# Kernel tuning notes

Measured on AMD Instinct MI355X. Metric: run time of the kernel, lower is better.

The kernel has to match this reference:

```python
import jax, jax.numpy as jnp
import numpy as np

N, E, M = 20000, 320000, 64
LOG2 = float(np.log(2.0))
INV_SQRT_M = 1.0 / float(np.sqrt(M))
PW_S = float(np.sqrt(1.0 / 5.0))   # path weight for 0e-output paths: sqrt(ir_out.dim / n_paths)
PW_V = float(np.sqrt(3.0 / 5.0))   # path weight for 1e-output paths
INV_SQRT3 = 1.0 / float(np.sqrt(3.0))
INV_SQRT2 = 1.0 / float(np.sqrt(2.0))


def ssp(x):  # ShiftedSoftPlus
    return jax.nn.softplus(x) - LOG2


def split(feat):
    return feat[:, :M], feat[:, M:].reshape(feat.shape[0], M, 3)


def e3_linear(feat, W0, b0, W1):
    # e3nn o3.Linear per irrep group, fan-in normalized; bias only on scalar (0e) irreps
    s, v = split(feat)
    s = s @ (W0 * INV_SQRT_M) + b0
    v = jnp.einsum('nui,uv->nvi', v, W1 * INV_SQRT_M)
    return jnp.concatenate([s, v.reshape(v.shape[0], 3 * M)], axis=-1)


def fcnet(h, Ws):
    # e3nn FullyConnectedNet: no biases, fan-in normalized, ssp between layers
    for i, W in enumerate(Ws):
        h = h @ (W * (1.0 / float(np.sqrt(W.shape[0]))))
        if i < len(Ws) - 1:
            h = ssp(h)
    return h


def setup_inputs() -> dict:
    key = jax.random.key(0)
    ks = jax.random.split(key, 24)
    r = lambda i, shape: jax.random.normal(ks[i], shape, dtype=jnp.float32)
    inp = {
        'x': r(0, (N, 4 * M)),
        'edge_index': jax.random.randint(ks[1], (2, E), 0, N, dtype=jnp.int64)
        if jax.config.jax_enable_x64 else jax.random.randint(ks[1], (2, E), 0, N),
        'edge_sh': r(2, (E, 4)),
        'edge_attr': r(3, (E, 64)),
        # linear_node_pre
        'W_pre0': r(4, (M, M)), 'b_pre0': jnp.zeros((M,), jnp.float32), 'W_pre1': r(5, (M, M)),
        # NormGate fc (plain torch nn.Linear with bias)
        'Wg1': r(6, (2 * M, 2 * M)) * 0.08, 'bg1': jnp.zeros((2 * M,), jnp.float32),
        'Wg2': r(7, (2 * M, 2 * M)) * 0.08, 'bg2': jnp.zeros((2 * M,), jnp.float32),
        # linear_node
        'Wn0': r(8, (M, M)), 'bn0': jnp.zeros((M,), jnp.float32), 'Wn1': r(9, (M, M)),
        # fc_node: [edge_attr_dim=64, 32, weight_numel=5*M]
        'Wf1': r(10, (64, 32)), 'Wf2': r(11, (32, 5 * M)),
        # layer_l0: [192, 32, 5*M]
        'Wl1': r(12, (192, 32)), 'Wl2': r(13, (32, 5 * M)),
        # linear_out
        'Wo0': r(14, (M, M)), 'bo0': jnp.zeros((M,), jnp.float32), 'Wo1': r(15, (M, M)),
    }
    return inp


def reference(x, edge_index, edge_sh, edge_attr,
              W_pre0, b_pre0, W_pre1, Wg1, bg1, Wg2, bg2,
              Wn0, bn0, Wn1, Wf1, Wf2, Wl1, Wl2, Wo0, bo0, Wo1):
    edge_dst, edge_src = edge_index[0], edge_index[1]

    # --- pre linear + edge invariants s0 ---
    pre_x = e3_linear(x, W_pre0, b_pre0, W_pre1)
    ps, pv = split(pre_x)
    # InnerProduct on 1e group (uuu, path weight 1/ir.dim): mean over m of elementwise product
    ip1 = jnp.einsum('eui,eui->eu', pv[edge_dst], pv[edge_src]) * (1.0 / 3.0)  # [E, M]
    s0 = jnp.concatenate([ps[edge_dst], ps[edge_dst], ip1], axis=-1)  # [E, 192]

    # --- NormGate ---
    xs, xv = split(x)
    norm_v = jnp.sqrt(jnp.sum(xv * xv, axis=-1) + 1e-12)  # [N, M]
    f0 = jnp.concatenate([xs, norm_v], axis=-1)  # [N, 2M]
    g = jax.nn.silu(f0 @ Wg1 + bg1) @ Wg2 + bg2  # [N, 2M]
    gated = xv * g[:, M:, None]
    xg = jnp.concatenate([g[:, :M], gated.reshape(N, 3 * M)], axis=-1)

    xg = e3_linear(xg, Wn0, bn0, Wn1)
    self_x = xg

    # --- per-edge tensor product weights ---
    w = (fcnet(edge_attr, [Wf1, Wf2]) * fcnet(s0, [Wl1, Wl2])).reshape(E, 5, M)

    # --- edge-wise equivariant tensor product (uvu, 5 paths) ---
    gs, gv = split(xg)
    es, ev = gs[edge_src], gv[edge_src]            # [E,M], [E,M,3]
    sh0, sh1 = edge_sh[:, 0], edge_sh[:, 1:4]      # [E], [E,3]

    out_s = PW_S * (w[:, 0] * es * sh0[:, None]
                    + w[:, 3] * jnp.einsum('eui,ei->eu', ev, sh1) * INV_SQRT3)
    cross = jnp.cross(ev, sh1[:, None, :])
    out_v = PW_V * (w[:, 1][:, :, None] * es[:, :, None] * sh1[:, None, :]
                    + w[:, 2][:, :, None] * ev * sh0[:, None, None]
                    + w[:, 4][:, :, None] * cross * INV_SQRT2)
    edge_feat = jnp.concatenate([out_s, out_v.reshape(E, 3 * M)], axis=-1)  # [E, 4M]

    # --- scatter aggregate to destination nodes ---
    out = jax.ops.segment_sum(edge_feat, edge_dst, num_segments=N)
    out = out + self_x  # irrep_in_node == irrep_out
    out = e3_linear(out, Wo0, bo0, Wo1)
    return out
```

## Files before the change

kernel.cpp:

```cpp
#include <hip/hip_runtime.h>
#include <math.h>

#define NNODE 20000
#define NEDGE 320000

__device__ __forceinline__ float sspf(float x) {
    return fmaxf(x, 0.f) + log1pf(expf(-fabsf(x))) - 0.6931471805599453f;
}

__device__ __forceinline__ float rl(float v, int l) {
    return __int_as_float(__builtin_amdgcn_readlane(__float_as_int(v), l));
}

__global__ __launch_bounds__(256) void k_e3lin(
    const float* __restrict__ in, const float* __restrict__ add,
    float* __restrict__ out,
    const float* __restrict__ W0, const float* __restrict__ b0,
    const float* __restrict__ W1, int nrows)
{
    __shared__ float sW0[64 * 64];
    __shared__ float sW1[64 * 64];
    __shared__ float sb0[64];
    __shared__ float srow[4][256];
    const int tid = threadIdx.x;
    for (int i = tid; i < 64 * 16; i += 256) {
        ((float4*)sW0)[i] = ((const float4*)W0)[i];
        ((float4*)sW1)[i] = ((const float4*)W1)[i];
    }
    if (tid < 64) sb0[tid] = b0[tid];
    __syncthreads();

    const int rr = tid >> 6;
    const int v  = tid & 63;
    for (int r0 = blockIdx.x * 4; r0 < nrows; r0 += gridDim.x * 4) {
        {
            int i = tid;
            int r = i >> 6, c = i & 63;
            int row = r0 + r;
            float4 val = make_float4(0.f, 0.f, 0.f, 0.f);
            if (row < nrows) {
                val = ((const float4*)(in + (size_t)row * 256))[c];
                if (add) {
                    float4 a = ((const float4*)(add + (size_t)row * 256))[c];
                    val.x += a.x; val.y += a.y; val.z += a.z; val.w += a.w;
                }
            }
            ((float4*)srow[r])[c] = val;
        }
        __syncthreads();

        int row = r0 + rr;
        if (row < nrows) {
            const float* rw = srow[rr];
            float s = 0.f, a0 = 0.f, a1 = 0.f, a2 = 0.f;
            #pragma unroll 16
            for (int u = 0; u < 64; ++u) {
                float w0 = sW0[u * 64 + v];
                float w1 = sW1[u * 64 + v];
                s  += rw[u] * w0;
                a0 += rw[64 + u * 3 + 0] * w1;
                a1 += rw[64 + u * 3 + 1] * w1;
                a2 += rw[64 + u * 3 + 2] * w1;
            }
            out[row * 256 + v]              = s  * 0.125f + sb0[v];
            out[row * 256 + 64 + v * 3 + 0] = a0 * 0.125f;
            out[row * 256 + 64 + v * 3 + 1] = a1 * 0.125f;
            out[row * 256 + 64 + v * 3 + 2] = a2 * 0.125f;
        }
        __syncthreads();
    }
}

__global__ __launch_bounds__(256) void k_gate(
    const float* __restrict__ x, float* __restrict__ xg,
    const float* __restrict__ Wg1, const float* __restrict__ bg1,
    const float* __restrict__ Wg2, const float* __restrict__ bg2,
    int nrows)
{
    __shared__ float sW1[128 * 128];
    __shared__ float sW2[128 * 128];
    __shared__ float sb1[128], sb2[128];
    __shared__ float srow[2][256];
    __shared__ float sf0[2][128];
    __shared__ float sh1[2][128];
    const int tid = threadIdx.x;
    for (int i = tid; i < 128 * 32; i += 256) {
        ((float4*)sW1)[i] = ((const float4*)Wg1)[i];
        ((float4*)sW2)[i] = ((const float4*)Wg2)[i];
    }
    if (tid < 128) { sb1[tid] = bg1[tid]; sb2[tid] = bg2[tid]; }
    __syncthreads();

    const int rr = tid >> 7;
    const int j  = tid & 127;
    for (int base = blockIdx.x * 2; base < nrows; base += gridDim.x * 2) {
        if (tid < 128) {
            int r = tid >> 6, c = tid & 63;
            int row = base + r;
            float4 v = make_float4(0.f, 0.f, 0.f, 0.f);
            if (row < nrows) v = ((const float4*)(x + (size_t)row * 256))[c];
            ((float4*)srow[r])[c] = v;
        }
        __syncthreads();
        {
            float f;
            if (j < 64) f = srow[rr][j];
            else {
                int u = j - 64;
                float v0 = srow[rr][64 + u * 3 + 0];
                float v1 = srow[rr][64 + u * 3 + 1];
                float v2 = srow[rr][64 + u * 3 + 2];
                f = sqrtf(v0 * v0 + v1 * v1 + v2 * v2 + 1e-12f);
            }
            sf0[rr][j] = f;
        }
        __syncthreads();
        {
            float acc = sb1[j];
            #pragma unroll 16
            for (int k = 0; k < 128; ++k) acc += sf0[rr][k] * sW1[k * 128 + j];
            sh1[rr][j] = acc / (1.f + expf(-acc));
        }
        __syncthreads();
        {
            float acc = sb2[j];
            #pragma unroll 16
            for (int k = 0; k < 128; ++k) acc += sh1[rr][k] * sW2[k * 128 + j];
            int row = base + rr;
            if (row < nrows) {
                if (j < 64) xg[row * 256 + j] = acc;
                else {
                    int u = j - 64;
                    xg[row * 256 + 64 + u * 3 + 0] = srow[rr][64 + u * 3 + 0] * acc;
                    xg[row * 256 + 64 + u * 3 + 1] = srow[rr][64 + u * 3 + 1] * acc;
                    xg[row * 256 + 64 + u * 3 + 2] = srow[rr][64 + u * 3 + 2] * acc;
                }
            }
        }
        __syncthreads();
    }
}

#define EPW 4
__global__ __launch_bounds__(1024, 1) void k_edge(
    const float* __restrict__ pre, const float* __restrict__ slf,
    const int* __restrict__ ei, const float* __restrict__ eshp,
    const float* __restrict__ ea,
    const float* __restrict__ Wf1, const float* __restrict__ Wf2,
    const float* __restrict__ Wl1, const float* __restrict__ Wl2,
    float* __restrict__ acc)
{
    __shared__ float sW1m[64 * 64];
    __shared__ float sW1b[64 * 64];
    __shared__ float sWf2[32 * 320];
    __shared__ float sWl2[32 * 320];
    const int tid = threadIdx.x;
    const float sc_f1 = 0.125f;
    const float sc_l1 = 0.07216878364870323f;
    const float sc_2  = 0.17677669529663687f;
    for (int i = tid; i < 64 * 64; i += 1024) {
        int u = i >> 6, c = i & 63, j = c & 31;
        if (c < 32) {
            sW1m[i] = Wf1[u * 32 + j] * sc_f1;
            sW1b[i] = 0.f;
        } else {
            sW1m[i] = (Wl1[u * 32 + j] + Wl1[(64 + u) * 32 + j]) * sc_l1;
            sW1b[i] = Wl1[(128 + u) * 32 + j] * sc_l1;
        }
    }
    for (int i = tid; i < 32 * 320; i += 1024) {
        sWf2[i] = Wf2[i] * sc_2;
        sWl2[i] = Wl2[i] * sc_2;
    }
    __syncthreads();

    const int lane  = tid & 63;
    const int wave  = tid >> 6;
    const int gwave = blockIdx.x * (blockDim.x >> 6) + wave;
    const int nwav  = gridDim.x * (blockDim.x >> 6);
    const bool lo   = (lane < 32);

    for (int base = gwave * EPW; base < NEDGE; base += nwav * EPW) {
        int dstv[EPW], srcv[EPW];
        float psd[EPW], ip1[EPW], eav[EPW];
        #pragma unroll
        for (int t = 0; t < EPW; ++t) {
            int e = base + t;
            int d = ei[e], s = ei[NEDGE + e];
            dstv[t] = d; srcv[t] = s;
            psd[t] = pre[d * 256 + lane];
            float pd0 = pre[d * 256 + 64 + lane * 3 + 0];
            float pd1 = pre[d * 256 + 64 + lane * 3 + 1];
            float pd2 = pre[d * 256 + 64 + lane * 3 + 2];
            float ps0 = pre[s * 256 + 64 + lane * 3 + 0];
            float ps1 = pre[s * 256 + 64 + lane * 3 + 1];
            float ps2 = pre[s * 256 + 64 + lane * 3 + 2];
            ip1[t] = (pd0 * ps0 + pd1 * ps1 + pd2 * ps2) * (1.f / 3.f);
            eav[t] = ea[e * 64 + lane];
        }

        float hacc[EPW] = {0.f, 0.f, 0.f, 0.f};
        #pragma unroll 16
        for (int uu = 0; uu < 64; ++uu) {
            float wm = sW1m[uu * 64 + lane];
            float wb = sW1b[uu * 64 + lane];
            #pragma unroll
            for (int t = 0; t < EPW; ++t) {
                float bA = rl(eav[t], uu);
                float bP = rl(psd[t], uu);
                float bI = rl(ip1[t], uu);
                float b1 = lo ? bA : bP;
                hacc[t] += b1 * wm + bI * wb;
            }
        }
        float hval[EPW];
        #pragma unroll
        for (int t = 0; t < EPW; ++t) hval[t] = sspf(hacc[t]);

        float aA[EPW][5], aB[EPW][5];
        #pragma unroll
        for (int t = 0; t < EPW; ++t)
            #pragma unroll
            for (int k = 0; k < 5; ++k) { aA[t][k] = 0.f; aB[t][k] = 0.f; }
        #pragma unroll 8
        for (int jj = 0; jj < 32; ++jj) {
            float wfa[5], wlb[5];
            #pragma unroll
            for (int k = 0; k < 5; ++k) {
                wfa[k] = sWf2[jj * 320 + k * 64 + lane];
                wlb[k] = sWl2[jj * 320 + k * 64 + lane];
            }
            #pragma unroll
            for (int t = 0; t < EPW; ++t) {
                float hA = rl(hval[t], jj);
                float hB = rl(hval[t], jj + 32);
                #pragma unroll
                for (int k = 0; k < 5; ++k) {
                    aA[t][k] += hA * wfa[k];
                    aB[t][k] += hB * wlb[k];
                }
            }
        }

        #pragma unroll
        for (int t = 0; t < EPW; ++t) {
            int e = base + t;
            float w0 = aA[t][0] * aB[t][0];
            float w1 = aA[t][1] * aB[t][1];
            float w2 = aA[t][2] * aB[t][2];
            float w3 = aA[t][3] * aB[t][3];
            float w4 = aA[t][4] * aB[t][4];
            int s = srcv[t];
            float es  = slf[s * 256 + lane];
            float ev0 = slf[s * 256 + 64 + lane * 3 + 0];
            float ev1 = slf[s * 256 + 64 + lane * 3 + 1];
            float ev2 = slf[s * 256 + 64 + lane * 3 + 2];
            float s0v = eshp[e * 4 + 0];
            float sx  = eshp[e * 4 + 1];
            float sy  = eshp[e * 4 + 2];
            float sz  = eshp[e * 4 + 3];
            float dotv = ev0 * sx + ev1 * sy + ev2 * sz;
            const float PW_S = 0.4472135954999579f;
            const float PW_V = 0.7745966692414834f;
            const float IS3  = 0.5773502691896258f;
            const float IS2  = 0.7071067811865476f;
            float outs = PW_S * (w0 * es * s0v + w3 * dotv * IS3);
            float cx = ev1 * sz - ev2 * sy;
            float cy = ev2 * sx - ev0 * sz;
            float cz = ev0 * sy - ev1 * sx;
            float ov0 = PW_V * (w1 * es * sx + w2 * ev0 * s0v + w4 * cx * IS2);
            float ov1 = PW_V * (w1 * es * sy + w2 * ev1 * s0v + w4 * cy * IS2);
            float ov2 = PW_V * (w1 * es * sz + w2 * ev2 * s0v + w4 * cz * IS2);
            int d = dstv[t];
            atomicAdd(&acc[d * 256 + lane], outs);
            atomicAdd(&acc[d * 256 + 64 + lane * 3 + 0], ov0);
            atomicAdd(&acc[d * 256 + 64 + lane * 3 + 1], ov1);
            atomicAdd(&acc[d * 256 + 64 + lane * 3 + 2], ov2);
        }
    }
}

extern "C" void kernel_launch(void* const* d_in, const int* in_sizes, int n_in,
                              void* d_out, int out_size, void* d_ws, size_t ws_size,
                              hipStream_t stream) {
    const float* x     = (const float*)d_in[0];
    const int*   ei    = (const int*)  d_in[1];
    const float* esh   = (const float*)d_in[2];
    const float* eattr = (const float*)d_in[3];
    const float* Wpre0 = (const float*)d_in[4];
    const float* bpre0 = (const float*)d_in[5];
    const float* Wpre1 = (const float*)d_in[6];
    const float* Wg1   = (const float*)d_in[7];
    const float* bg1   = (const float*)d_in[8];
    const float* Wg2   = (const float*)d_in[9];
    const float* bg2   = (const float*)d_in[10];
    const float* Wn0   = (const float*)d_in[11];
    const float* bn0   = (const float*)d_in[12];
    const float* Wn1   = (const float*)d_in[13];
    const float* Wf1   = (const float*)d_in[14];
    const float* Wf2   = (const float*)d_in[15];
    const float* Wl1   = (const float*)d_in[16];
    const float* Wl2   = (const float*)d_in[17];
    const float* Wo0   = (const float*)d_in[18];
    const float* bo0   = (const float*)d_in[19];
    const float* Wo1   = (const float*)d_in[20];
    float* out = (float*)d_out;
    float* ws  = (float*)d_ws;

    float* pre = ws;
    float* xg  = ws + (size_t)NNODE * 256;
    float* slf = ws + (size_t)NNODE * 256 * 2;
    float* acc = ws + (size_t)NNODE * 256 * 3;

    hipMemsetAsync(acc, 0, (size_t)NNODE * 256 * sizeof(float), stream);
    k_e3lin<<<1280, 256, 0, stream>>>(x,  nullptr, pre, Wpre0, bpre0, Wpre1, NNODE);
    k_gate <<<512,  256, 0, stream>>>(x,  xg, Wg1, bg1, Wg2, bg2, NNODE);
    k_e3lin<<<1280, 256, 0, stream>>>(xg, nullptr, slf, Wn0, bn0, Wn1, NNODE);
    k_edge <<<256, 1024, 0, stream>>>(pre, slf, ei, esh, eattr, Wf1, Wf2, Wl1, Wl2, acc);
    k_e3lin<<<1280, 256, 0, stream>>>(acc, slf, out, Wo0, bo0, Wo1, NNODE);
}
```

Before: 1.269 ms.

## Replace readlane broadcasts with LDS staging, pack weights, halve edges per wave

The edge kernel no longer broadcasts per-lane inputs with readlane. Each wave writes its inputs and hidden activations to per-wave LDS buffers and reads them back as broadcast loads. Weight tables are repacked into float2/float4 so each lane fetches its coefficients with vector LDS loads. Edges per wave drop from 4 to 2 and launch bounds now request more waves per SIMD, trading per-wave reuse for occupancy and latency hiding. The write-then-read of sIN and sH within a wave relies on wave-level execution ordering with no explicit barrier.

```diff
diff --git a/kernel.cpp b/kernel.cpp
--- a/kernel.cpp
+++ b/kernel.cpp
@@ -6,10 +6,6 @@
 
 __device__ __forceinline__ float sspf(float x) {
     return fmaxf(x, 0.f) + log1pf(expf(-fabsf(x))) - 0.6931471805599453f;
-}
-
-__device__ __forceinline__ float rl(float v, int l) {
-    return __int_as_float(__builtin_amdgcn_readlane(__float_as_int(v), l));
 }
 
 __global__ __launch_bounds__(256) void k_e3lin(
@@ -141,8 +137,8 @@
     }
 }
 
-#define EPW 4
-__global__ __launch_bounds__(1024, 1) void k_edge(
+#define EPW 2
+__global__ __launch_bounds__(1024, 4) void k_edge(
     const float* __restrict__ pre, const float* __restrict__ slf,
     const int* __restrict__ ei, const float* __restrict__ eshp,
     const float* __restrict__ ea,
@@ -150,72 +146,79 @@
     const float* __restrict__ Wl1, const float* __restrict__ Wl2,
     float* __restrict__ acc)
 {
-    __shared__ float sW1m[64 * 64];
-    __shared__ float sW1b[64 * 64];
-    __shared__ float sWf2[32 * 320];
-    __shared__ float sWl2[32 * 320];
+    __shared__ float2 sW1mb[64 * 64];
+    __shared__ float4 sW2a[32 * 64];
+    __shared__ float4 sW2b[32 * 64];
+    __shared__ float2 sW2c[32 * 64];
+    __shared__ float  sIN[16][EPW][192];
+    __shared__ float  sH [16][EPW][64];
     const int tid = threadIdx.x;
     const float sc_f1 = 0.125f;
     const float sc_l1 = 0.07216878364870323f;
     const float sc_2  = 0.17677669529663687f;
     for (int i = tid; i < 64 * 64; i += 1024) {
         int u = i >> 6, c = i & 63, j = c & 31;
+        float wm, wb;
         if (c < 32) {
-            sW1m[i] = Wf1[u * 32 + j] * sc_f1;
-            sW1b[i] = 0.f;
+            wm = Wf1[u * 32 + j] * sc_f1;
+            wb = 0.f;
         } else {
-            sW1m[i] = (Wl1[u * 32 + j] + Wl1[(64 + u) * 32 + j]) * sc_l1;
-            sW1b[i] = Wl1[(128 + u) * 32 + j] * sc_l1;
-        }
-    }
-    for (int i = tid; i < 32 * 320; i += 1024) {
-        sWf2[i] = Wf2[i] * sc_2;
-        sWl2[i] = Wl2[i] * sc_2;
+            wm = (Wl1[u * 32 + j] + Wl1[(64 + u) * 32 + j]) * sc_l1;
+            wb = Wl1[(128 + u) * 32 + j] * sc_l1;
+        }
+        sW1mb[i] = make_float2(wm, wb);
+    }
+    for (int i = tid; i < 32 * 64; i += 1024) {
+        int jj = i >> 6, col = i & 63;
+        const float* f2 = Wf2 + jj * 320 + col;
+        const float* l2 = Wl2 + jj * 320 + col;
+        sW2a[i] = make_float4(f2[0] * sc_2, f2[64] * sc_2, f2[128] * sc_2, f2[192] * sc_2);
+        sW2b[i] = make_float4(l2[0] * sc_2, l2[64] * sc_2, l2[128] * sc_2, l2[192] * sc_2);
+        sW2c[i] = make_float2(f2[256] * sc_2, l2[256] * sc_2);
     }
     __syncthreads();
 
     const int lane  = tid & 63;
-    const int wave  = tid >> 6;
-    const int gwave = blockIdx.x * (blockDim.x >> 6) + wave;
+    const int w     = tid >> 6;
+    const int gwave = blockIdx.x * (blockDim.x >> 6) + w;
     const int nwav  = gridDim.x * (blockDim.x >> 6);
-    const bool lo   = (lane < 32);
-
-    for (int base = gwave * EPW; base < NEDGE; base += nwav * EPW) {
+    const float* inb = &sIN[w][0][(lane >> 5) << 6];
+
+    for (int base0 = gwave * EPW; base0 < NEDGE; base0 += nwav * EPW) {
+        const int base = __builtin_amdgcn_readfirstlane(base0);
         int dstv[EPW], srcv[EPW];
-        float psd[EPW], ip1[EPW], eav[EPW];
         #pragma unroll
         for (int t = 0; t < EPW; ++t) {
             int e = base + t;
             int d = ei[e], s = ei[NEDGE + e];
             dstv[t] = d; srcv[t] = s;
-            psd[t] = pre[d * 256 + lane];
+            float psd = pre[d * 256 + lane];
             float pd0 = pre[d * 256 + 64 + lane * 3 + 0];
             float pd1 = pre[d * 256 + 64 + lane * 3 + 1];
             float pd2 = pre[d * 256 + 64 + lane * 3 + 2];
             float ps0 = pre[s * 256 + 64 + lane * 3 + 0];
             float ps1 = pre[s * 256 + 64 + lane * 3 + 1];
             float ps2 = pre[s * 256 + 64 + lane * 3 + 2];
-            ip1[t] = (pd0 * ps0 + pd1 * ps1 + pd2 * ps2) * (1.f / 3.f);
-            eav[t] = ea[e * 64 + lane];
-        }
-
-        float hacc[EPW] = {0.f, 0.f, 0.f, 0.f};
+            float ip1 = (pd0 * ps0 + pd1 * ps1 + pd2 * ps2) * (1.f / 3.f);
+            float eav = ea[e * 64 + lane];
+            sIN[w][t][lane]       = eav;
+            sIN[w][t][64 + lane]  = psd;
+            sIN[w][t][128 + lane] = ip1;
+        }
+
+        float hacc[EPW] = {0.f, 0.f};
         #pragma unroll 16
         for (int uu = 0; uu < 64; ++uu) {
-            float wm = sW1m[uu * 64 + lane];
-            float wb = sW1b[uu * 64 + lane];
+            float2 wmb = sW1mb[uu * 64 + lane];
             #pragma unroll
             for (int t = 0; t < EPW; ++t) {
-                float bA = rl(eav[t], uu);
-                float bP = rl(psd[t], uu);
-                float bI = rl(ip1[t], uu);
-                float b1 = lo ? bA : bP;
-                hacc[t] += b1 * wm + bI * wb;
-            }
-        }
-        float hval[EPW];
+                float b1 = inb[t * 192 + uu];
+                float bI = sIN[w][t][128 + uu];
+                hacc[t] += b1 * wmb.x + bI * wmb.y;
+            }
+        }
         #pragma unroll
-        for (int t = 0; t < EPW; ++t) hval[t] = sspf(hacc[t]);
+        for (int t = 0; t < EPW; ++t) sH[w][t][lane] = sspf(hacc[t]);
 
         float aA[EPW][5], aB[EPW][5];
         #pragma unroll
@@ -224,21 +227,19 @@
             for (int k = 0; k < 5; ++k) { aA[t][k] = 0.f; aB[t][k] = 0.f; }
         #pragma unroll 8
         for (int jj = 0; jj < 32; ++jj) {
-            float wfa[5], wlb[5];
-            #pragma unroll
-            for (int k = 0; k < 5; ++k) {
-                wfa[k] = sWf2[jj * 320 + k * 64 + lane];
-                wlb[k] = sWl2[jj * 320 + k * 64 + lane];
-            }
+            float4 wa = sW2a[jj * 64 + lane];
+            float4 wb = sW2b[jj * 64 + lane];
+            float2 wc = sW2c[jj * 64 + lane];
             #pragma unroll
             for (int t = 0; t < EPW; ++t) {
-                float hA = rl(hval[t], jj);
-                float hB = rl(hval[t], jj + 32);
-                #pragma unroll
-                for (int k = 0; k < 5; ++k) {
-                    aA[t][k] += hA * wfa[k];
-                    aB[t][k] += hB * wlb[k];
-                }
+                float hA = sH[w][t][jj];
+                float hB = sH[w][t][32 + jj];
+                aA[t][0] += hA * wa.x; aA[t][1] += hA * wa.y;
+                aA[t][2] += hA * wa.z; aA[t][3] += hA * wa.w;
+                aA[t][4] += hA * wc.x;
+                aB[t][0] += hB * wb.x; aB[t][1] += hB * wb.y;
+                aB[t][2] += hB * wb.z; aB[t][3] += hB * wb.w;
+                aB[t][4] += hB * wc.y;
             }
         }
 
```

Result: faster. 1.204 ms (-5.2%).
